# Optimization experiments

Measured on AMD Instinct MI355X. Metric: run time of the kernel, lower is better.

The kernel has to match this reference:

```python
import jax, jax.numpy as jnp
import numpy as np

N_NODES = 65536
IN_DIM = 512
OUT_DIM = 512
N_EDGES = 524288
BN_EPS = 1e-5
NORM_EPS = 1e-6


def setup_inputs() -> dict:
    key = jax.random.key(0)
    k1, k2, k3, k4 = jax.random.split(key, 4)
    features = jax.random.normal(k1, (N_NODES, IN_DIM), dtype=jnp.float32)
    edge_index = jax.random.randint(k2, (2, N_EDGES), 0, N_NODES, dtype=jnp.int64)
    # torch Linear weight layout: [out_features, in_features] with in = 2*IN_DIM
    W = jax.random.normal(k3, (OUT_DIM, 2 * IN_DIM), dtype=jnp.float32) * (1.0 / np.sqrt(2 * IN_DIM))
    b = jax.random.normal(k4, (OUT_DIM,), dtype=jnp.float32) * 0.01
    gamma = jnp.ones((OUT_DIM,), dtype=jnp.float32)
    beta = jnp.zeros((OUT_DIM,), dtype=jnp.float32)
    running_mean = jnp.zeros((OUT_DIM,), dtype=jnp.float32)
    running_var = jnp.ones((OUT_DIM,), dtype=jnp.float32)
    return {
        "features": features,
        "edge_index": edge_index,
        "W": W,
        "b": b,
        "gamma": gamma,
        "beta": beta,
        "running_mean": running_mean,
        "running_var": running_var,
    }


def reference(features, edge_index, W, b, gamma, beta, running_mean, running_var):
    sources = edge_index[0]
    targets = edge_index[1]
    # scatter-sum of neighbor (target) features into source rows  [N, D]
    aggregated = jax.ops.segment_sum(features[targets], sources, num_segments=N_NODES)
    out = jnp.concatenate([features, aggregated], axis=1)  # [N, 2D]
    out = out @ W.T + b  # [N, OUT_DIM]
    out = jax.nn.relu(out)
    # BatchNorm1d (eval mode, running stats)
    out = (out - running_mean) * jax.lax.rsqrt(running_var + BN_EPS) * gamma + beta
    # dropout is identity in inference
    out = out / (jnp.linalg.norm(out, axis=1, keepdims=True) + NORM_EPS)
    return out
```

## Files before the change

### kernel.cpp

```cpp
#include <hip/hip_runtime.h>
#include <hip/hip_bf16.h>

#define N_NODES 65536
#define DIM 512
#define N_EDGES 524288
#define BN_EPS 1e-5f
#define NORM_EPS 1e-6f

typedef __attribute__((ext_vector_type(8))) short short8;
typedef __attribute__((ext_vector_type(4))) float f32x4;

static __device__ __forceinline__ unsigned f2bf(float f) {
    union { float f; unsigned u; } c; c.f = f;
    unsigned u = c.u;
    return (u + 0x7fffu + ((u >> 16) & 1u)) >> 16;
}
static __device__ __forceinline__ float bf16lo(unsigned u) {
    union { unsigned u; float f; } c; c.u = u << 16; return c.f;
}
static __device__ __forceinline__ float bf16hi(unsigned u) {
    union { unsigned u; float f; } c; c.u = u & 0xffff0000u; return c.f;
}
static __device__ __forceinline__ uint4 pack8(float4 a, float4 b) {
    uint4 o;
    o.x = f2bf(a.x) | (f2bf(a.y) << 16);
    o.y = f2bf(a.z) | (f2bf(a.w) << 16);
    o.z = f2bf(b.x) | (f2bf(b.y) << 16);
    o.w = f2bf(b.z) | (f2bf(b.w) << 16);
    return o;
}

__global__ void convert_kernel(const float* __restrict__ src,
                               unsigned short* __restrict__ dst, int n8) {
    int i = blockIdx.x * blockDim.x + threadIdx.x;
    if (i < n8) {
        const float4* s = (const float4*)src + i * 2;
        float4 f0 = s[0], f1 = s[1];
        ((uint4*)dst)[i] = pack8(f0, f1);
    }
}

__global__ void hist_kernel(const int* __restrict__ src, int* __restrict__ counts) {
    int e = blockIdx.x * blockDim.x + threadIdx.x;
    if (e < N_EDGES) atomicAdd(&counts[src[e]], 1);
}

__global__ void scan_partial(const int* __restrict__ counts, int* __restrict__ partials) {
    __shared__ int ws[4];
    int t = threadIdx.x;
    int v = counts[blockIdx.x * 256 + t];
#pragma unroll
    for (int d = 1; d < 64; d <<= 1) v += __shfl_xor(v, d);
    if ((t & 63) == 0) ws[t >> 6] = v;
    __syncthreads();
    if (t == 0) partials[blockIdx.x] = ws[0] + ws[1] + ws[2] + ws[3];
}

__global__ void scan_base(int* __restrict__ partials) {
    __shared__ int lds[256];
    int t = threadIdx.x;
    int v = partials[t];
    lds[t] = v;
    __syncthreads();
    for (int d = 1; d < 256; d <<= 1) {
        int mine = lds[t];
        int add = (t >= d) ? lds[t - d] : 0;
        __syncthreads();
        lds[t] = mine + add;
        __syncthreads();
    }
    partials[t] = lds[t] - v;
}

__global__ void scan_final(const int* __restrict__ counts,
                           const int* __restrict__ partials,
                           int* __restrict__ offsets, int* __restrict__ cursor) {
    __shared__ int lds[256];
    int t = threadIdx.x, b = blockIdx.x;
    int v = counts[b * 256 + t];
    lds[t] = v;
    __syncthreads();
    for (int d = 1; d < 256; d <<= 1) {
        int mine = lds[t];
        int add = (t >= d) ? lds[t - d] : 0;
        __syncthreads();
        lds[t] = mine + add;
        __syncthreads();
    }
    int excl = lds[t] - v + partials[b];
    offsets[b * 256 + t] = excl;
    cursor[b * 256 + t] = excl;
    if (b == 255 && t == 255) offsets[N_NODES] = excl + v;
}

__global__ void scatter_kernel(const int* __restrict__ src, const int* __restrict__ tgt,
                               int* __restrict__ cursor, int* __restrict__ sortedT) {
    int e = blockIdx.x * blockDim.x + threadIdx.x;
    if (e < N_EDGES) {
        int s = src[e];
        int pos = atomicAdd(&cursor[s], 1);
        sortedT[pos] = tgt[e];
    }
}

__global__ void aggregate_kernel(const unsigned short* __restrict__ Xb,
                                 const int* __restrict__ offsets,
                                 const int* __restrict__ sortedT,
                                 unsigned short* __restrict__ agg) {
    int wave = (blockIdx.x * blockDim.x + threadIdx.x) >> 6;
    int lane = threadIdx.x & 63;
    if (wave >= N_NODES) return;
    int beg = offsets[wave], end = offsets[wave + 1];
    float a[8] = {0.f, 0.f, 0.f, 0.f, 0.f, 0.f, 0.f, 0.f};
    const uint4* F = (const uint4*)Xb;
    for (int i = beg; i < end; ++i) {
        int t = sortedT[i];
        uint4 v = F[t * 64 + lane];
        a[0] += bf16lo(v.x); a[1] += bf16hi(v.x);
        a[2] += bf16lo(v.y); a[3] += bf16hi(v.y);
        a[4] += bf16lo(v.z); a[5] += bf16hi(v.z);
        a[6] += bf16lo(v.w); a[7] += bf16hi(v.w);
    }
    uint4 o;
    o.x = f2bf(a[0]) | (f2bf(a[1]) << 16);
    o.y = f2bf(a[2]) | (f2bf(a[3]) << 16);
    o.z = f2bf(a[4]) | (f2bf(a[5]) << 16);
    o.w = f2bf(a[6]) | (f2bf(a[7]) << 16);
    ((uint4*)agg)[wave * 64 + lane] = o;
}

__global__ __launch_bounds__(512, 4) void fused_gemm_norm_kernel(
        const unsigned short* __restrict__ Xb,
        const unsigned short* __restrict__ agg,
        const unsigned short* __restrict__ Wb,
        const float* __restrict__ bias,
        const float* __restrict__ gamma,
        const float* __restrict__ beta,
        const float* __restrict__ rmean,
        const float* __restrict__ rvar,
        float* __restrict__ out) {
    __shared__ uint4 Alds[512];
    __shared__ uint4 Blds[4096];
    __shared__ float ssm[64][8];

    const int t = threadIdx.x;
    const int m0 = blockIdx.x * 64;
    const int w = t >> 6, L = t & 63;
    const int ml = L & 15, quad = L >> 4;
    const int wn = w * 64;

    f32x4 acc[4][4];
#pragma unroll
    for (int mi = 0; mi < 4; ++mi)
#pragma unroll
        for (int ni = 0; ni < 4; ++ni)
            acc[mi][ni] = (f32x4){0.f, 0.f, 0.f, 0.f};

    for (int kt = 0; kt < 16; ++kt) {
        const unsigned short* Asrc = (kt < 8) ? (Xb + kt * 64) : (agg + (kt - 8) * 64);
        __syncthreads();
        {
            int c = t;
            int r = c >> 3, pp = c & 7;
            int p = pp ^ (r & 7);
            const unsigned short* ga = Asrc + (m0 + r) * 512 + p * 8;
            char* la = (char*)Alds + (t & 448) * 16;
            __builtin_amdgcn_global_load_lds(
                (const __attribute__((address_space(1))) unsigned int*)ga,
                (__attribute__((address_space(3))) unsigned int*)la, 16, 0, 0);
        }
#pragma unroll
        for (int j = 0; j < 8; ++j) {
            int c = j * 512 + t;
            int r = c >> 3, pp = c & 7;
            int p = pp ^ (r & 7);
            const unsigned short* gb = Wb + r * 1024 + kt * 64 + p * 8;
            char* lb = (char*)Blds + (j * 512 + (t & 448)) * 16;
            __builtin_amdgcn_global_load_lds(
                (const __attribute__((address_space(1))) unsigned int*)gb,
                (__attribute__((address_space(3))) unsigned int*)lb, 16, 0, 0);
        }
        __syncthreads();
#pragma unroll
        for (int kc = 0; kc < 2; ++kc) {
            int g = kc * 4 + quad;
            short8 a[4], b[4];
#pragma unroll
            for (int mi = 0; mi < 4; ++mi) {
                int ra = mi * 16 + ml;
                a[mi] = *(const short8*)&Alds[ra * 8 + (g ^ (ra & 7))];
                int rb = wn + mi * 16 + ml;
                b[mi] = *(const short8*)&Blds[rb * 8 + (g ^ (rb & 7))];
            }
#pragma unroll
            for (int mi = 0; mi < 4; ++mi)
#pragma unroll
                for (int ni = 0; ni < 4; ++ni)
                    acc[mi][ni] = __builtin_amdgcn_mfma_f32_16x16x32_bf16(
                        a[mi], b[ni], acc[mi][ni], 0, 0, 0);
        }
    }

    float bi[4], sc[4], sh[4];
#pragma unroll
    for (int ni = 0; ni < 4; ++ni) {
        int col = wn + ni * 16 + ml;
        bi[ni] = bias[col];
        sc[ni] = gamma[col] * __frsqrt_rn(rvar[col] + BN_EPS);
        sh[ni] = beta[col] - rmean[col] * sc[ni];
    }
    float ss[4][4];
#pragma unroll
    for (int mi = 0; mi < 4; ++mi)
#pragma unroll
        for (int r = 0; r < 4; ++r)
            ss[mi][r] = 0.f;
#pragma unroll
    for (int mi = 0; mi < 4; ++mi)
#pragma unroll
        for (int ni = 0; ni < 4; ++ni)
#pragma unroll
            for (int r = 0; r < 4; ++r) {
                float v = fmaxf(acc[mi][ni][r] + bi[ni], 0.f) * sc[ni] + sh[ni];
                acc[mi][ni][r] = v;
                ss[mi][r] += v * v;
            }
#pragma unroll
    for (int mi = 0; mi < 4; ++mi)
#pragma unroll
        for (int r = 0; r < 4; ++r) {
#pragma unroll
            for (int d = 1; d < 16; d <<= 1)
                ss[mi][r] += __shfl_xor(ss[mi][r], d);
        }
    if (ml == 0) {
#pragma unroll
        for (int mi = 0; mi < 4; ++mi)
#pragma unroll
            for (int r = 0; r < 4; ++r)
                ssm[mi * 16 + quad * 4 + r][w] = ss[mi][r];
    }
    __syncthreads();
#pragma unroll
    for (int mi = 0; mi < 4; ++mi)
#pragma unroll
        for (int r = 0; r < 4; ++r) {
            int rl = mi * 16 + quad * 4 + r;
            const float4* sp = (const float4*)ssm[rl];
            float4 s0 = sp[0], s1 = sp[1];
            float tot = s0.x + s0.y + s0.z + s0.w + s1.x + s1.y + s1.z + s1.w;
            float inv = 1.f / (sqrtf(tot) + NORM_EPS);
            int m = m0 + rl;
#pragma unroll
            for (int ni = 0; ni < 4; ++ni)
                out[m * 512 + wn + ni * 16 + ml] = acc[mi][ni][r] * inv;
        }
}

extern "C" void kernel_launch(void* const* d_in, const int* in_sizes, int n_in,
                              void* d_out, int out_size, void* d_ws, size_t ws_size,
                              hipStream_t stream) {
    const float* features = (const float*)d_in[0];
    const int* edges      = (const int*)d_in[1];
    const float* W        = (const float*)d_in[2];
    const float* bias     = (const float*)d_in[3];
    const float* gamma    = (const float*)d_in[4];
    const float* beta     = (const float*)d_in[5];
    const float* rmean    = (const float*)d_in[6];
    const float* rvar     = (const float*)d_in[7];
    float* out = (float*)d_out;

    char* ws = (char*)d_ws;
    int* counts   = (int*)(ws);
    int* offsets  = (int*)(ws + 0x100000);
    int* cursor   = (int*)(ws + 0x200000);
    int* partials = (int*)(ws + 0x280000);
    int* sortedT  = (int*)(ws + 0x300000);
    unsigned short* Wb  = (unsigned short*)(ws + 0x500000);
    unsigned short* Xb  = (unsigned short*)(ws + 0x600000);
    unsigned short* agg = (unsigned short*)(ws + 0x4600000);

    const int* src = edges;
    const int* tgt = edges + N_EDGES;

    hipMemsetAsync(counts, 0, N_NODES * sizeof(int), stream);
    hist_kernel<<<N_EDGES / 256, 256, 0, stream>>>(src, counts);
    scan_partial<<<256, 256, 0, stream>>>(counts, partials);
    scan_base<<<1, 256, 0, stream>>>(partials);
    scan_final<<<256, 256, 0, stream>>>(counts, partials, offsets, cursor);
    scatter_kernel<<<N_EDGES / 256, 256, 0, stream>>>(src, tgt, cursor, sortedT);
    convert_kernel<<<(N_NODES * DIM / 8) / 256, 256, 0, stream>>>(features, Xb, N_NODES * DIM / 8);
    convert_kernel<<<(DIM * 2 * DIM / 8) / 256, 256, 0, stream>>>(W, Wb, DIM * 2 * DIM / 8);
    aggregate_kernel<<<N_NODES / 4, 256, 0, stream>>>(Xb, offsets, sortedT, agg);
    fused_gemm_norm_kernel<<<N_NODES / 64, 512, 0, stream>>>(
        Xb, agg, Wb, bias, gamma, beta, rmean, rvar, out);
}
```

Measured before the change: 451.4 us.

## Double-buffer GEMM LDS tiles and unroll edge gather in aggregation

The fused GEMM kernel now double-buffers its A and B LDS tiles, issuing async global-to-LDS loads for the next K tile while MFMAs run on the current one, with one barrier per iteration. Each wave now loads only its own B rows, and the norm scratch reuses the A buffer. Launch bounds drop to 2 blocks per SM because LDS use doubles. The aggregation kernel unrolls the edge loop by 4 with two accumulator sets to raise memory-level parallelism. The tradeoff is lower occupancy in the GEMM kernel.

```diff
diff --git a/kernel.cpp b/kernel.cpp
--- a/kernel.cpp
+++ b/kernel.cpp
@@ -101,6 +101,13 @@
         int pos = atomicAdd(&cursor[s], 1);
         sortedT[pos] = tgt[e];
     }
+}
+
+static __device__ __forceinline__ void acc8(float* a, uint4 v) {
+    a[0] += bf16lo(v.x); a[1] += bf16hi(v.x);
+    a[2] += bf16lo(v.y); a[3] += bf16hi(v.y);
+    a[4] += bf16lo(v.z); a[5] += bf16hi(v.z);
+    a[6] += bf16lo(v.w); a[7] += bf16hi(v.w);
 }
 
 __global__ void aggregate_kernel(const unsigned short* __restrict__ Xb,
@@ -112,15 +119,31 @@
     if (wave >= N_NODES) return;
     int beg = offsets[wave], end = offsets[wave + 1];
     float a[8] = {0.f, 0.f, 0.f, 0.f, 0.f, 0.f, 0.f, 0.f};
+    float b[8] = {0.f, 0.f, 0.f, 0.f, 0.f, 0.f, 0.f, 0.f};
     const uint4* F = (const uint4*)Xb;
-    for (int i = beg; i < end; ++i) {
-        int t = sortedT[i];
-        uint4 v = F[t * 64 + lane];
-        a[0] += bf16lo(v.x); a[1] += bf16hi(v.x);
-        a[2] += bf16lo(v.y); a[3] += bf16hi(v.y);
-        a[4] += bf16lo(v.z); a[5] += bf16hi(v.z);
-        a[6] += bf16lo(v.w); a[7] += bf16hi(v.w);
-    }
+    int i = beg;
+    for (; i + 4 <= end; i += 4) {
+        int t0 = sortedT[i], t1 = sortedT[i + 1], t2 = sortedT[i + 2], t3 = sortedT[i + 3];
+        uint4 v0 = F[t0 * 64 + lane];
+        uint4 v1 = F[t1 * 64 + lane];
+        uint4 v2 = F[t2 * 64 + lane];
+        uint4 v3 = F[t3 * 64 + lane];
+        acc8(a, v0); acc8(b, v1); acc8(a, v2); acc8(b, v3);
+    }
+    if (i + 2 <= end) {
+        int t0 = sortedT[i], t1 = sortedT[i + 1];
+        uint4 v0 = F[t0 * 64 + lane];
+        uint4 v1 = F[t1 * 64 + lane];
+        acc8(a, v0); acc8(b, v1);
+        i += 2;
+    }
+    if (i < end) {
+        int t0 = sortedT[i];
+        uint4 v0 = F[t0 * 64 + lane];
+        acc8(a, v0);
+    }
+#pragma unroll
+    for (int k = 0; k < 8; ++k) a[k] += b[k];
     uint4 o;
     o.x = f2bf(a[0]) | (f2bf(a[1]) << 16);
     o.y = f2bf(a[2]) | (f2bf(a[3]) << 16);
@@ -129,7 +152,7 @@
     ((uint4*)agg)[wave * 64 + lane] = o;
 }
 
-__global__ __launch_bounds__(512, 4) void fused_gemm_norm_kernel(
+__global__ __launch_bounds__(512, 2) void fused_gemm_norm_kernel(
         const unsigned short* __restrict__ Xb,
         const unsigned short* __restrict__ agg,
         const unsigned short* __restrict__ Wb,
@@ -139,9 +162,9 @@
         const float* __restrict__ rmean,
         const float* __restrict__ rvar,
         float* __restrict__ out) {
-    __shared__ uint4 Alds[512];
-    __shared__ uint4 Blds[4096];
-    __shared__ float ssm[64][8];
+    __shared__ uint4 Abuf[2][512];
+    __shared__ uint4 Bbuf[2][4096];
+    float (*ssm)[8] = reinterpret_cast<float (*)[8]>(&Abuf[0][0]);
 
     const int t = threadIdx.x;
     const int m0 = blockIdx.x * 64;
@@ -149,38 +172,43 @@
     const int ml = L & 15, quad = L >> 4;
     const int wn = w * 64;
 
-    f32x4 acc[4][4];
-#pragma unroll
-    for (int mi = 0; mi < 4; ++mi)
-#pragma unroll
-        for (int ni = 0; ni < 4; ++ni)
-            acc[mi][ni] = (f32x4){0.f, 0.f, 0.f, 0.f};
-
-    for (int kt = 0; kt < 16; ++kt) {
+    auto stage = [&](int buf, int kt) {
         const unsigned short* Asrc = (kt < 8) ? (Xb + kt * 64) : (agg + (kt - 8) * 64);
-        __syncthreads();
         {
-            int c = t;
-            int r = c >> 3, pp = c & 7;
+            int r = t >> 3, pp = t & 7;
             int p = pp ^ (r & 7);
             const unsigned short* ga = Asrc + (m0 + r) * 512 + p * 8;
-            char* la = (char*)Alds + (t & 448) * 16;
+            char* la = (char*)&Abuf[buf][t & 448];
             __builtin_amdgcn_global_load_lds(
                 (const __attribute__((address_space(1))) unsigned int*)ga,
                 (__attribute__((address_space(3))) unsigned int*)la, 16, 0, 0);
         }
 #pragma unroll
         for (int j = 0; j < 8; ++j) {
-            int c = j * 512 + t;
-            int r = c >> 3, pp = c & 7;
-            int p = pp ^ (r & 7);
-            const unsigned short* gb = Wb + r * 1024 + kt * 64 + p * 8;
-            char* lb = (char*)Blds + (j * 512 + (t & 448)) * 16;
+            int c = j * 64 + L;
+            int rl = c >> 3, pp = c & 7;
+            int p = pp ^ (rl & 7);
+            const unsigned short* gb = Wb + (wn + rl) * 1024 + kt * 64 + p * 8;
+            char* lb = (char*)&Bbuf[buf][w * 512 + j * 64];
             __builtin_amdgcn_global_load_lds(
                 (const __attribute__((address_space(1))) unsigned int*)gb,
                 (__attribute__((address_space(3))) unsigned int*)lb, 16, 0, 0);
         }
-        __syncthreads();
+    };
+
+    f32x4 acc[4][4];
+#pragma unroll
+    for (int mi = 0; mi < 4; ++mi)
+#pragma unroll
+        for (int ni = 0; ni < 4; ++ni)
+            acc[mi][ni] = (f32x4){0.f, 0.f, 0.f, 0.f};
+
+    stage(0, 0);
+    __syncthreads();
+
+    int cur = 0;
+    for (int kt = 0; kt < 16; ++kt) {
+        if (kt < 15) stage(cur ^ 1, kt + 1);
 #pragma unroll
         for (int kc = 0; kc < 2; ++kc) {
             int g = kc * 4 + quad;
@@ -188,9 +216,9 @@
 #pragma unroll
             for (int mi = 0; mi < 4; ++mi) {
                 int ra = mi * 16 + ml;
-                a[mi] = *(const short8*)&Alds[ra * 8 + (g ^ (ra & 7))];
-                int rb = wn + mi * 16 + ml;
-                b[mi] = *(const short8*)&Blds[rb * 8 + (g ^ (rb & 7))];
+                a[mi] = *(const short8*)&Abuf[cur][ra * 8 + (g ^ (ra & 7))];
+                int rl = mi * 16 + ml;
+                b[mi] = *(const short8*)&Bbuf[cur][w * 512 + rl * 8 + (g ^ (rl & 7))];
             }
 #pragma unroll
             for (int mi = 0; mi < 4; ++mi)
@@ -199,6 +227,8 @@
                     acc[mi][ni] = __builtin_amdgcn_mfma_f32_16x16x32_bf16(
                         a[mi], b[ni], acc[mi][ni], 0, 0, 0);
         }
+        __syncthreads();
+        cur ^= 1;
     }
 
     float bi[4], sc[4], sh[4];
```

After: 495.0 us. 1.1x slower.
